# Optimization experiments

Measured on AMD Instinct MI355X. Metric: run time of the kernel, lower is better.

Reference implementation:

```python
import jax, jax.numpy as jnp
import numpy as np

B, S, E, H = 8, 1024, 1024, 16
DK = E // H  # = n_wires = 64


def setup_inputs() -> dict:
    key = jax.random.key(0)
    k1, k2, k3 = jax.random.split(key, 3)
    x = jax.random.normal(k1, (B, S, E), dtype=jnp.float32)
    # trainable per-wire RX angles (shared across tokens and heads, as in QLayer)
    theta = jax.random.normal(k2, (DK,), dtype=jnp.float32)
    # combine_heads: nn.Linear(E, E, bias=False) -> weight [E, E], y = x @ W.T
    W_combine = (jax.random.normal(k3, (E, E), dtype=jnp.float32) / np.float32(np.sqrt(E)))
    return {"x": x, "theta": theta, "W_combine": W_combine}


def reference(x, theta, W_combine):
    # Quantum projection: per wire, RX(x_i) then RX(theta_i) on |0>, measure PauliZ.
    # RX(a)RX(b) = RX(a+b); <Z> of RX(a)|0> = cos(a)  =>  proj = cos(x + theta).
    b, s, e = x.shape
    xh = x.reshape(b, s, H, DK)            # [B, S, H, DK]
    proj = jnp.cos(xh + theta)             # product-state circuit, fully vectorized
    qkv = proj.transpose(0, 2, 1, 3)       # [B, H, S, DK]; q = k = v = proj

    scale = jnp.float32(1.0 / np.sqrt(DK))
    scores = jnp.einsum('bhqd,bhkd->bhqk', qkv, qkv) * scale  # [B, H, S, S]
    attn = jax.nn.softmax(scores, axis=-1)  # dropout disabled (eval / p=0)
    out = jnp.einsum('bhqk,bhkd->bhqd', attn, qkv)            # [B, H, S, DK]
    out = out.transpose(0, 2, 1, 3).reshape(b, s, e)          # [B, S, E]
    return out @ W_combine.T
```

## Files before the change

### kernel.cpp

```cpp
#include <hip/hip_runtime.h>
#include <hip/hip_bf16.h>
#include <stdint.h>

typedef float  f32x4   __attribute__((ext_vector_type(4)));
typedef float  f32x16  __attribute__((ext_vector_type(16)));
typedef __bf16 bf16x8  __attribute__((ext_vector_type(8)));
typedef __bf16 bf16x4  __attribute__((ext_vector_type(4)));

static constexpr int NB = 8, NS = 1024, NE = 1024, NH = 16;

#define MFMA16(a, b, c) __builtin_amdgcn_mfma_f32_16x16x32_bf16((a), (b), (c), 0, 0, 0)
#define MFMA32(a, b, c) __builtin_amdgcn_mfma_f32_32x32x16_bf16((a), (b), (c), 0, 0, 0)

__device__ __forceinline__ void gload_lds16(const void* g, void* l) {
    __builtin_amdgcn_global_load_lds(
        (const __attribute__((address_space(1))) void*)g,
        (__attribute__((address_space(3))) void*)l, 16, 0, 0);
}

__device__ __forceinline__ uint32_t cvt_pk_bf16(float lo, float hi) {
    uint32_t r;
    asm("v_cvt_pk_bf16_f32 %0, %1, %2" : "=v"(r) : "v"(lo), "v"(hi));
    return r;
}
__device__ __forceinline__ void pl32swap(uint32_t& a, uint32_t& b) {
    asm volatile("v_permlane32_swap_b32 %0, %1" : "+v"(a), "+v"(b));
}
__device__ __forceinline__ float exp2_raw(float x) {
    float r;
    asm("v_exp_f32 %0, %1" : "=v"(r) : "v"(x));
    return r;
}

__global__ __launch_bounds__(256) void k_proj(const float* __restrict__ x,
                                              const float* __restrict__ theta,
                                              __bf16* __restrict__ proj,
                                              __bf16* __restrict__ projT) {
    __shared__ float sm[64][65];
    const int bid  = blockIdx.x;
    const int bh   = bid >> 4;
    const int st0  = (bid & 15) << 6;
    const int b    = bh >> 4, h = bh & 15;
    const int t    = threadIdx.x;
    const int srow = t >> 2;
    const int j4   = t & 3;

    const float* xrow = x + ((size_t)(b * NS + st0 + srow)) * NE + h * 64;
    __bf16* prow = proj + ((size_t)bh * NS + st0 + srow) * 64;

#pragma unroll
    for (int k = 0; k < 4; ++k) {
        const int d = k * 16 + j4 * 4;
        float4 xv = *(const float4*)(xrow + d);
        float4 tv = *(const float4*)(theta + d);
        float c0 = __cosf(xv.x + tv.x);
        float c1 = __cosf(xv.y + tv.y);
        float c2 = __cosf(xv.z + tv.z);
        float c3 = __cosf(xv.w + tv.w);
        bf16x4 pv = {(__bf16)c0, (__bf16)c1, (__bf16)c2, (__bf16)c3};
        *(bf16x4*)(prow + d) = pv;
        sm[d + 0][srow] = c0;
        sm[d + 1][srow] = c1;
        sm[d + 2][srow] = c2;
        sm[d + 3][srow] = c3;
    }
    __syncthreads();

    const int drow = t >> 2;
    bf16x8 o0, o1;
#pragma unroll
    for (int i = 0; i < 8; ++i) {
        o0[i] = (__bf16)sm[drow][j4 * 16 + i];
        o1[i] = (__bf16)sm[drow][j4 * 16 + 8 + i];
    }
    __bf16* dst = projT + ((size_t)bh * 64 + drow) * NS + st0 + j4 * 16;
    *(bf16x8*)dst = o0;
    *(bf16x8*)(dst + 8) = o1;
}

__global__ __launch_bounds__(256) void k_cvtW(const float* __restrict__ W,
                                              __bf16* __restrict__ Wb) {
    const int i = (blockIdx.x * 256 + threadIdx.x) * 4;
    float4 v = *(const float4*)(W + i);
    bf16x4 o = {(__bf16)v.x, (__bf16)v.y, (__bf16)v.z, (__bf16)v.w};
    *(bf16x4*)(Wb + i) = o;
}

__global__ __launch_bounds__(256, 2) void k_attn(const __bf16* __restrict__ proj,
                                                 const __bf16* __restrict__ projT,
                                                 __bf16* __restrict__ attn_out) {
    __shared__ __align__(16) char smem[49152];
    __bf16* const smK0 = (__bf16*)(smem);
    __bf16* const smV0 = (__bf16*)(smem + 8192);
    __bf16* const smK1 = (__bf16*)(smem + 16384);
    __bf16* const smV1 = (__bf16*)(smem + 24576);
    __bf16* const smK2 = (__bf16*)(smem + 32768);
    __bf16* const smV2 = (__bf16*)(smem + 40960);

    const int bid  = blockIdx.x;
    const int bh   = (bid & 7) + 8 * ((bid >> 3) & 15);
    const int qblk = bid >> 7;
    const int t    = threadIdx.x;
    const int w    = t >> 6;
    const int lane = t & 63;
    const int hi   = lane >> 5;
    const int l5   = lane & 31;
    const int l7   = l5 & 7;
    const int qw   = qblk * 256 + w * 64;
    const int b    = bh >> 4, h = bh & 15;

    const __bf16* P  = proj  + (size_t)bh * NS * 64;
    const __bf16* PT = projT + (size_t)bh * 64 * NS;

    const float csc = 0.18033688f;

    bf16x8 bq[2][4];
#pragma unroll
    for (int q01 = 0; q01 < 2; ++q01)
#pragma unroll
        for (int d = 0; d < 4; ++d)
            bq[q01][d] = *(const bf16x8*)(P + (size_t)(qw + q01 * 32 + l5) * 64 + d * 16 + hi * 8);

    int roff[4];
#pragma unroll
    for (int d = 0; d < 4; ++d) roff[d] = l5 * 64 + ((d * 2 + hi) ^ l7) * 8;

    const int srow  = t >> 3;
    const int sjsrc = (t & 7) ^ (srow & 7);
    char* const sdK0 = (char*)smK0 + t * 16;
    char* const sdV0 = (char*)smV0 + t * 16;
    char* const sdK1 = (char*)smK1 + t * 16;
    char* const sdV1 = (char*)smV1 + t * 16;
    char* const sdK2 = (char*)smK2 + t * 16;
    char* const sdV2 = (char*)smV2 + t * 16;

#define STAGE(kvoff, dk, dv)                                                           \
    do {                                                                               \
        gload_lds16(P  + (size_t)((kvoff) + srow)      * 64 + sjsrc * 8, (dk));        \
        gload_lds16(P  + (size_t)((kvoff) + 32 + srow) * 64 + sjsrc * 8, (dk) + 4096); \
        gload_lds16(PT + (size_t)srow        * NS + (kvoff) + sjsrc * 8, (dv));        \
        gload_lds16(PT + (size_t)(32 + srow) * NS + (kvoff) + sjsrc * 8, (dv) + 4096); \
    } while (0)

    f32x16 acc0[2], acc1[2];
#pragma unroll
    for (int dt = 0; dt < 2; ++dt) {
        acc0[dt] = (f32x16){0.f,0.f,0.f,0.f,0.f,0.f,0.f,0.f,0.f,0.f,0.f,0.f,0.f,0.f,0.f,0.f};
        acc1[dt] = (f32x16){0.f,0.f,0.f,0.f,0.f,0.f,0.f,0.f,0.f,0.f,0.f,0.f,0.f,0.f,0.f,0.f};
    }
    float rs0 = 0.f, rs1 = 0.f;

    auto computeTile = [&](const __bf16* kB, const __bf16* vB) {
#pragma unroll
        for (int kt = 0; kt < 2; ++kt) {
            bf16x8 ak[4];
#pragma unroll
            for (int d = 0; d < 4; ++d)
                ak[d] = *(const bf16x8*)(kB + roff[d] + kt * 2048);

            f32x16 st0 = (f32x16){0.f,0.f,0.f,0.f,0.f,0.f,0.f,0.f,0.f,0.f,0.f,0.f,0.f,0.f,0.f,0.f};
            f32x16 st1 = (f32x16){0.f,0.f,0.f,0.f,0.f,0.f,0.f,0.f,0.f,0.f,0.f,0.f,0.f,0.f,0.f,0.f};
            __builtin_amdgcn_s_setprio(1);
#pragma unroll
            for (int d = 0; d < 4; ++d) {
                st0 = MFMA32(ak[d], bq[0][d], st0);
                st1 = MFMA32(ak[d], bq[1][d], st1);
            }
            __builtin_amdgcn_s_setprio(0);

            uint32_t c0[8], c1[8];
            {
                float p[16];
#pragma unroll
                for (int r = 0; r < 16; ++r) p[r] = exp2_raw(st0[r] * csc);
                rs0 += (((p[0] + p[1]) + (p[2] + p[3])) + ((p[4] + p[5]) + (p[6] + p[7]))) +
                       (((p[8] + p[9]) + (p[10] + p[11])) + ((p[12] + p[13]) + (p[14] + p[15])));
#pragma unroll
                for (int j = 0; j < 8; ++j) c0[j] = cvt_pk_bf16(p[2 * j], p[2 * j + 1]);
            }
            {
                float p[16];
#pragma unroll
                for (int r = 0; r < 16; ++r) p[r] = exp2_raw(st1[r] * csc);
                rs1 += (((p[0] + p[1]) + (p[2] + p[3])) + ((p[4] + p[5]) + (p[6] + p[7]))) +
                       (((p[8] + p[9]) + (p[10] + p[11])) + ((p[12] + p[13]) + (p[14] + p[15])));
#pragma unroll
                for (int j = 0; j < 8; ++j) c1[j] = cvt_pk_bf16(p[2 * j], p[2 * j + 1]);
            }
            pl32swap(c0[0], c0[2]); pl32swap(c0[1], c0[3]);
            pl32swap(c0[4], c0[6]); pl32swap(c0[5], c0[7]);
            pl32swap(c1[0], c1[2]); pl32swap(c1[1], c1[3]);
            pl32swap(c1[4], c1[6]); pl32swap(c1[5], c1[7]);

#pragma unroll
            for (int half = 0; half < 2; ++half) {
                const int ks = kt * 2 + half;
                union U4 { uint32_t u[4]; bf16x8 v; };
                U4 f0, f1;
#pragma unroll
                for (int j = 0; j < 4; ++j) {
                    f0.u[j] = c0[half * 4 + j];
                    f1.u[j] = c1[half * 4 + j];
                }
                __builtin_amdgcn_s_setprio(1);
#pragma unroll
                for (int dt = 0; dt < 2; ++dt) {
                    bf16x8 av = *(const bf16x8*)(vB + roff[ks] + dt * 2048);
                    acc0[dt] = MFMA32(av, f0.v, acc0[dt]);
                    acc1[dt] = MFMA32(av, f1.v, acc1[dt]);
                }
                __builtin_amdgcn_s_setprio(0);
            }
        }
    };

#define PHASE(IT, CUR, NXT, WAITN)                                        \
    do {                                                                  \
        asm volatile("s_waitcnt vmcnt(" #WAITN ")" ::: "memory");         \
        __builtin_amdgcn_sched_barrier(0);                                \
        __builtin_amdgcn_s_barrier();                                     \
        __builtin_amdgcn_sched_barrier(0);                                \
        if ((IT) < 14) STAGE(((IT) + 2) * 64, sdK##NXT, sdV##NXT);        \
        computeTile(smK##CUR, smV##CUR);                                  \
    } while (0)

    STAGE(0, sdK0, sdV0);
    STAGE(64, sdK1, sdV1);

#pragma unroll 1
    for (int g3 = 0; g3 < 5; ++g3) {
        const int it0 = g3 * 3;
        PHASE(it0 + 0, 0, 2, 4);
        PHASE(it0 + 1, 1, 0, 4);
        PHASE(it0 + 2, 2, 1, 4);
    }
    PHASE(15, 0, 2, 0);

#undef PHASE
#undef STAGE

    __builtin_amdgcn_sched_barrier(0);
    __builtin_amdgcn_s_barrier();

    float* const epw = (float*)smem + w * (32 * 33);
    const int orow = lane >> 1;
    const int ohalf = lane & 1;

#pragma unroll
    for (int q01 = 0; q01 < 2; ++q01) {
        float rs = (q01 == 0) ? rs0 : rs1;
        rs += __shfl_xor(rs, 32);
        const float inv = 1.0f / rs;
#pragma unroll
        for (int dt = 0; dt < 2; ++dt) {
            const f32x16 a = (q01 == 0) ? acc0[dt] : acc1[dt];
#pragma unroll
            for (int r = 0; r < 16; ++r)
                epw[l5 * 33 + (r & 3) + 8 * (r >> 2) + 4 * hi] = a[r] * inv;
            bf16x8 o0, o1;
#pragma unroll
            for (int i = 0; i < 8; ++i) {
                o0[i] = (__bf16)(epw[orow * 33 + ohalf * 16 + i]);
                o1[i] = (__bf16)(epw[orow * 33 + ohalf * 16 + 8 + i]);
            }
            __bf16* dst = attn_out +
                ((size_t)b * NS + qblk * 256 + w * 64 + q01 * 32 + orow) * NE +
                h * 64 + dt * 32 + ohalf * 16;
            *(bf16x8*)dst = o0;
            *(bf16x8*)(dst + 8) = o1;
        }
    }
}

__global__ __launch_bounds__(256) void k_gemm(const __bf16* __restrict__ A,
                                              const __bf16* __restrict__ Bw,
                                              float* __restrict__ C) {
    constexpr int K = 1024, N = 1024;
    __shared__ __bf16 As[128 * 32];
    __shared__ __bf16 Bs[128 * 32];

    const int t = threadIdx.x;
    const int lane = t & 63, w = t >> 6;
    const int g = lane >> 4, c = lane & 15;
    const int wr = w >> 1, wc = w & 1;
    const size_t row0 = (size_t)blockIdx.x * 128;
    const size_t col0 = (size_t)blockIdx.y * 128;

    const char* Ag = (const char*)(A + row0 * K);
    const char* Bg = (const char*)(Bw + col0 * K);
    char* AsB = (char*)As;
    char* BsB = (char*)Bs;
    const int srow  = t >> 2;
    const int sbyte = (t & 3) * 16;

    f32x4 acc[4][4];
#pragma unroll
    for (int m = 0; m < 4; ++m)
#pragma unroll
        for (int n = 0; n < 4; ++n) acc[m][n] = (f32x4){0.f, 0.f, 0.f, 0.f};

    for (int kb = 0; kb < K; kb += 32) {
        gload_lds16(Ag + (size_t)srow * (K * 2) + kb * 2 + sbyte, AsB + t * 16);
        gload_lds16(Ag + (size_t)(srow + 64) * (K * 2) + kb * 2 + sbyte, AsB + 4096 + t * 16);
        gload_lds16(Bg + (size_t)srow * (K * 2) + kb * 2 + sbyte, BsB + t * 16);
        gload_lds16(Bg + (size_t)(srow + 64) * (K * 2) + kb * 2 + sbyte, BsB + 4096 + t * 16);
        __syncthreads();

        bf16x8 a[4], b[4];
#pragma unroll
        for (int m = 0; m < 4; ++m)
            a[m] = *(const bf16x8*)(As + (wr * 64 + m * 16 + c) * 32 + g * 8);
#pragma unroll
        for (int n = 0; n < 4; ++n)
            b[n] = *(const bf16x8*)(Bs + (wc * 64 + n * 16 + c) * 32 + g * 8);
#pragma unroll
        for (int m = 0; m < 4; ++m)
#pragma unroll
            for (int n = 0; n < 4; ++n) acc[m][n] = MFMA16(a[m], b[n], acc[m][n]);
        __syncthreads();
    }

#pragma unroll
    for (int m = 0; m < 4; ++m)
#pragma unroll
        for (int n = 0; n < 4; ++n)
#pragma unroll
            for (int r = 0; r < 4; ++r)
                C[(row0 + wr * 64 + m * 16 + 4 * g + r) * N + col0 + wc * 64 + n * 16 + c] =
                    acc[m][n][r];
}

extern "C" void kernel_launch(void* const* d_in, const int* in_sizes, int n_in,
                              void* d_out, int out_size, void* d_ws, size_t ws_size,
                              hipStream_t stream) {
    const float* x     = (const float*)d_in[0];
    const float* theta = (const float*)d_in[1];
    const float* W     = (const float*)d_in[2];
    float* out = (float*)d_out;

    char* ws = (char*)d_ws;
    __bf16* proj  = (__bf16*)(ws);
    __bf16* projT = (__bf16*)(ws + 16777216);
    __bf16* Wb    = (__bf16*)(ws + 33554432);
    __bf16* ao    = (__bf16*)(ws + 35651584);

    k_proj<<<NB * NH * (NS / 64), 256, 0, stream>>>(x, theta, proj, projT);
    k_cvtW<<<(NE * NE / 4) / 256, 256, 0, stream>>>(W, Wb);
    k_attn<<<NB * NH * 4, 256, 0, stream>>>(proj, projT, ao);
    dim3 gg(NB * NS / 128, NE / 128);
    k_gemm<<<gg, 256, 0, stream>>>(ao, Wb, out);
}
```

Before: 99.39 us.

## Double KV tile to 128 rows and switch to double-buffered LDS staging

Each attention pipeline step now stages 128 keys/values instead of 64, using two 32 KB LDS buffers instead of three 16 KB buffers. The V tile layout and swizzle offsets are widened to match. The hand-tuned vmcnt waits and triple-buffer rotation are replaced with a simpler stage-next/compute-current loop separated by __syncthreads. The intent is to halve the number of barriers and grow the work per sync, at the cost of a shallower prefetch and a full memory wait at every barrier. LDS use per block also rises to 64 KB.

```diff
diff --git a/kernel.cpp b/kernel.cpp
--- a/kernel.cpp
+++ b/kernel.cpp
@@ -89,13 +89,11 @@
 __global__ __launch_bounds__(256, 2) void k_attn(const __bf16* __restrict__ proj,
                                                  const __bf16* __restrict__ projT,
                                                  __bf16* __restrict__ attn_out) {
-    __shared__ __align__(16) char smem[49152];
+    __shared__ __align__(16) char smem[65536];
     __bf16* const smK0 = (__bf16*)(smem);
-    __bf16* const smV0 = (__bf16*)(smem + 8192);
-    __bf16* const smK1 = (__bf16*)(smem + 16384);
-    __bf16* const smV1 = (__bf16*)(smem + 24576);
-    __bf16* const smK2 = (__bf16*)(smem + 32768);
-    __bf16* const smV2 = (__bf16*)(smem + 40960);
+    __bf16* const smV0 = (__bf16*)(smem + 16384);
+    __bf16* const smK1 = (__bf16*)(smem + 32768);
+    __bf16* const smV1 = (__bf16*)(smem + 49152);
 
     const int bid  = blockIdx.x;
     const int bh   = (bid & 7) + 8 * ((bid >> 3) & 15);
@@ -121,25 +119,31 @@
         for (int d = 0; d < 4; ++d)
             bq[q01][d] = *(const bf16x8*)(P + (size_t)(qw + q01 * 32 + l5) * 64 + d * 16 + hi * 8);
 
-    int roff[4];
-#pragma unroll
-    for (int d = 0; d < 4; ++d) roff[d] = l5 * 64 + ((d * 2 + hi) ^ l7) * 8;
-
-    const int srow  = t >> 3;
-    const int sjsrc = (t & 7) ^ (srow & 7);
-    char* const sdK0 = (char*)smK0 + t * 16;
-    char* const sdV0 = (char*)smV0 + t * 16;
-    char* const sdK1 = (char*)smK1 + t * 16;
-    char* const sdV1 = (char*)smV1 + t * 16;
-    char* const sdK2 = (char*)smK2 + t * 16;
-    char* const sdV2 = (char*)smV2 + t * 16;
-
-#define STAGE(kvoff, dk, dv)                                                           \
-    do {                                                                               \
-        gload_lds16(P  + (size_t)((kvoff) + srow)      * 64 + sjsrc * 8, (dk));        \
-        gload_lds16(P  + (size_t)((kvoff) + 32 + srow) * 64 + sjsrc * 8, (dk) + 4096); \
-        gload_lds16(PT + (size_t)srow        * NS + (kvoff) + sjsrc * 8, (dv));        \
-        gload_lds16(PT + (size_t)(32 + srow) * NS + (kvoff) + sjsrc * 8, (dv) + 4096); \
+    int roffK[4], roffV[8];
+#pragma unroll
+    for (int d = 0; d < 4; ++d) roffK[d] = l5 * 64 + ((d * 2 + hi) ^ l7) * 8;
+#pragma unroll
+    for (int ks = 0; ks < 8; ++ks) roffV[ks] = l5 * 128 + ((ks * 2 + hi) ^ l7) * 8;
+
+    const int srowK = t >> 3;
+    const int sjK   = (t & 7) ^ (srowK & 7);
+    const int srowV = t >> 4;
+    const int sjV   = (t & 15) ^ (srowV & 7);
+    char* const dK0 = (char*)smK0 + t * 16;
+    char* const dV0 = (char*)smV0 + t * 16;
+    char* const dK1 = (char*)smK1 + t * 16;
+    char* const dV1 = (char*)smV1 + t * 16;
+
+#define STAGE(kvoff, dk, dv)                                                             \
+    do {                                                                                 \
+        gload_lds16(P + (size_t)((kvoff) + srowK) * 64 + sjK * 8, (dk));                 \
+        gload_lds16(P + (size_t)((kvoff) + 32 + srowK) * 64 + sjK * 8, (dk) + 4096);     \
+        gload_lds16(P + (size_t)((kvoff) + 64 + srowK) * 64 + sjK * 8, (dk) + 8192);     \
+        gload_lds16(P + (size_t)((kvoff) + 96 + srowK) * 64 + sjK * 8, (dk) + 12288);    \
+        gload_lds16(PT + (size_t)srowV * NS + (kvoff) + sjV * 8, (dv));                  \
+        gload_lds16(PT + (size_t)(16 + srowV) * NS + (kvoff) + sjV * 8, (dv) + 4096);    \
+        gload_lds16(PT + (size_t)(32 + srowV) * NS + (kvoff) + sjV * 8, (dv) + 8192);    \
+        gload_lds16(PT + (size_t)(48 + srowV) * NS + (kvoff) + sjV * 8, (dv) + 12288);   \
     } while (0)
 
     f32x16 acc0[2], acc1[2];
@@ -152,11 +156,11 @@
 
     auto computeTile = [&](const __bf16* kB, const __bf16* vB) {
 #pragma unroll
-        for (int kt = 0; kt < 2; ++kt) {
+        for (int kt = 0; kt < 4; ++kt) {
             bf16x8 ak[4];
 #pragma unroll
             for (int d = 0; d < 4; ++d)
-                ak[d] = *(const bf16x8*)(kB + roff[d] + kt * 2048);
+                ak[d] = *(const bf16x8*)(kB + roffK[d] + kt * 2048);
 
             f32x16 st0 = (f32x16){0.f,0.f,0.f,0.f,0.f,0.f,0.f,0.f,0.f,0.f,0.f,0.f,0.f,0.f,0.f,0.f};
             f32x16 st1 = (f32x16){0.f,0.f,0.f,0.f,0.f,0.f,0.f,0.f,0.f,0.f,0.f,0.f,0.f,0.f,0.f,0.f};
@@ -205,7 +209,7 @@
                 __builtin_amdgcn_s_setprio(1);
 #pragma unroll
                 for (int dt = 0; dt < 2; ++dt) {
-                    bf16x8 av = *(const bf16x8*)(vB + roff[ks] + dt * 2048);
+                    bf16x8 av = *(const bf16x8*)(vB + roffV[ks] + dt * 4096);
                     acc0[dt] = MFMA32(av, f0.v, acc0[dt]);
                     acc1[dt] = MFMA32(av, f1.v, acc1[dt]);
                 }
@@ -214,33 +218,19 @@
         }
     };
 
-#define PHASE(IT, CUR, NXT, WAITN)                                        \
-    do {                                                                  \
-        asm volatile("s_waitcnt vmcnt(" #WAITN ")" ::: "memory");         \
-        __builtin_amdgcn_sched_barrier(0);                                \
-        __builtin_amdgcn_s_barrier();                                     \
-        __builtin_amdgcn_sched_barrier(0);                                \
-        if ((IT) < 14) STAGE(((IT) + 2) * 64, sdK##NXT, sdV##NXT);        \
-        computeTile(smK##CUR, smV##CUR);                                  \
-    } while (0)
-
-    STAGE(0, sdK0, sdV0);
-    STAGE(64, sdK1, sdV1);
+    STAGE(0, dK0, dV0);
+    __syncthreads();
 
 #pragma unroll 1
-    for (int g3 = 0; g3 < 5; ++g3) {
-        const int it0 = g3 * 3;
-        PHASE(it0 + 0, 0, 2, 4);
-        PHASE(it0 + 1, 1, 0, 4);
-        PHASE(it0 + 2, 2, 1, 4);
-    }
-    PHASE(15, 0, 2, 0);
-
-#undef PHASE
+    for (int it2 = 0; it2 < 4; ++it2) {
+        STAGE((2 * it2 + 1) * 128, dK1, dV1);
+        computeTile(smK0, smV0);
+        __syncthreads();
+        if (it2 < 3) STAGE((2 * it2 + 2) * 128, dK0, dV0);
+        computeTile(smK1, smV1);
+        __syncthreads();
+    }
 #undef STAGE
-
-    __builtin_amdgcn_sched_barrier(0);
-    __builtin_amdgcn_s_barrier();
 
     float* const epw = (float*)smem + w * (32 * 33);
     const int orow = lane >> 1;
```

Result: slower. 114.8 us (+15.5%).

## Double-buffer GEMM with swizzled 64-wide K tiles; simplify attention pipeline to two buffers

Applied to the files above, without the earlier changes.

The output-projection GEMM now uses double-buffered 128x64 LDS tiles with an XOR swizzle, staging the next K tile while computing the current one. This is meant to hide global-load latency and cut barrier count and LDS bank conflicts. The attention kernel drops from a three-buffer, vmcnt-controlled pipeline to a two-buffer scheme synchronized with __syncthreads, which shrinks its LDS footprint but waits on all outstanding loads at every barrier. The k_cvtW launch is also reordered ahead of k_proj.

```diff
diff --git a/kernel.cpp b/kernel.cpp
--- a/kernel.cpp
+++ b/kernel.cpp
@@ -89,13 +89,11 @@
 __global__ __launch_bounds__(256, 2) void k_attn(const __bf16* __restrict__ proj,
                                                  const __bf16* __restrict__ projT,
                                                  __bf16* __restrict__ attn_out) {
-    __shared__ __align__(16) char smem[49152];
+    __shared__ __align__(16) char smem[32768];
     __bf16* const smK0 = (__bf16*)(smem);
     __bf16* const smV0 = (__bf16*)(smem + 8192);
     __bf16* const smK1 = (__bf16*)(smem + 16384);
     __bf16* const smV1 = (__bf16*)(smem + 24576);
-    __bf16* const smK2 = (__bf16*)(smem + 32768);
-    __bf16* const smV2 = (__bf16*)(smem + 40960);
 
     const int bid  = blockIdx.x;
     const int bh   = (bid & 7) + 8 * ((bid >> 3) & 15);
@@ -127,12 +125,10 @@
 
     const int srow  = t >> 3;
     const int sjsrc = (t & 7) ^ (srow & 7);
-    char* const sdK0 = (char*)smK0 + t * 16;
-    char* const sdV0 = (char*)smV0 + t * 16;
-    char* const sdK1 = (char*)smK1 + t * 16;
-    char* const sdV1 = (char*)smV1 + t * 16;
-    char* const sdK2 = (char*)smK2 + t * 16;
-    char* const sdV2 = (char*)smV2 + t * 16;
+    char* const dK0 = (char*)smK0 + t * 16;
+    char* const dV0 = (char*)smV0 + t * 16;
+    char* const dK1 = (char*)smK1 + t * 16;
+    char* const dV1 = (char*)smV1 + t * 16;
 
 #define STAGE(kvoff, dk, dv)                                                           \
     do {                                                                               \
@@ -214,33 +210,19 @@
         }
     };
 
-#define PHASE(IT, CUR, NXT, WAITN)                                        \
-    do {                                                                  \
-        asm volatile("s_waitcnt vmcnt(" #WAITN ")" ::: "memory");         \
-        __builtin_amdgcn_sched_barrier(0);                                \
-        __builtin_amdgcn_s_barrier();                                     \
-        __builtin_amdgcn_sched_barrier(0);                                \
-        if ((IT) < 14) STAGE(((IT) + 2) * 64, sdK##NXT, sdV##NXT);        \
-        computeTile(smK##CUR, smV##CUR);                                  \
-    } while (0)
-
-    STAGE(0, sdK0, sdV0);
-    STAGE(64, sdK1, sdV1);
+    STAGE(0, dK0, dV0);
+    __syncthreads();
 
 #pragma unroll 1
-    for (int g3 = 0; g3 < 5; ++g3) {
-        const int it0 = g3 * 3;
-        PHASE(it0 + 0, 0, 2, 4);
-        PHASE(it0 + 1, 1, 0, 4);
-        PHASE(it0 + 2, 2, 1, 4);
-    }
-    PHASE(15, 0, 2, 0);
-
-#undef PHASE
+    for (int it2 = 0; it2 < 8; ++it2) {
+        STAGE((2 * it2 + 1) * 64, dK1, dV1);
+        computeTile(smK0, smV0);
+        __syncthreads();
+        if (it2 < 7) STAGE((2 * it2 + 2) * 64, dK0, dV0);
+        computeTile(smK1, smV1);
+        __syncthreads();
+    }
 #undef STAGE
-
-    __builtin_amdgcn_sched_barrier(0);
-    __builtin_amdgcn_s_barrier();
 
     float* const epw = (float*)smem + w * (32 * 33);
     const int orow = lane >> 1;
@@ -272,12 +254,12 @@
     }
 }
 
-__global__ __launch_bounds__(256) void k_gemm(const __bf16* __restrict__ A,
-                                              const __bf16* __restrict__ Bw,
-                                              float* __restrict__ C) {
+__global__ __launch_bounds__(256, 2) void k_gemm(const __bf16* __restrict__ A,
+                                                 const __bf16* __restrict__ Bw,
+                                                 float* __restrict__ C) {
     constexpr int K = 1024, N = 1024;
-    __shared__ __bf16 As[128 * 32];
-    __shared__ __bf16 Bs[128 * 32];
+    __shared__ __align__(16) __bf16 As[2][128 * 64];
+    __shared__ __align__(16) __bf16 Bs[2][128 * 64];
 
     const int t = threadIdx.x;
     const int lane = t & 63, w = t >> 6;
@@ -286,12 +268,22 @@
     const size_t row0 = (size_t)blockIdx.x * 128;
     const size_t col0 = (size_t)blockIdx.y * 128;
 
-    const char* Ag = (const char*)(A + row0 * K);
-    const char* Bg = (const char*)(Bw + col0 * K);
-    char* AsB = (char*)As;
-    char* BsB = (char*)Bs;
-    const int srow  = t >> 2;
-    const int sbyte = (t & 3) * 16;
+    const __bf16* Ag = A  + row0 * K;
+    const __bf16* Bg = Bw + col0 * K;
+
+    const int srow = t >> 3;
+    const int sj   = (t & 7) ^ (srow & 7);
+
+#define GSTAGE(kb, buf)                                                           \
+    do {                                                                          \
+        _Pragma("unroll")                                                         \
+        for (int p = 0; p < 4; ++p) {                                             \
+            gload_lds16(Ag + (size_t)(p * 32 + srow) * K + (kb) + sj * 8,         \
+                        (char*)&As[buf][0] + p * 4096 + t * 16);                  \
+            gload_lds16(Bg + (size_t)(p * 32 + srow) * K + (kb) + sj * 8,         \
+                        (char*)&Bs[buf][0] + p * 4096 + t * 16);                  \
+        }                                                                         \
+    } while (0)
 
     f32x4 acc[4][4];
 #pragma unroll
@@ -299,26 +291,40 @@
 #pragma unroll
         for (int n = 0; n < 4; ++n) acc[m][n] = (f32x4){0.f, 0.f, 0.f, 0.f};
 
-    for (int kb = 0; kb < K; kb += 32) {
-        gload_lds16(Ag + (size_t)srow * (K * 2) + kb * 2 + sbyte, AsB + t * 16);
-        gload_lds16(Ag + (size_t)(srow + 64) * (K * 2) + kb * 2 + sbyte, AsB + 4096 + t * 16);
-        gload_lds16(Bg + (size_t)srow * (K * 2) + kb * 2 + sbyte, BsB + t * 16);
-        gload_lds16(Bg + (size_t)(srow + 64) * (K * 2) + kb * 2 + sbyte, BsB + 4096 + t * 16);
+    const int c7 = c & 7;
+
+    auto computeBuf = [&](int buf) {
+#pragma unroll
+        for (int ks = 0; ks < 2; ++ks) {
+            bf16x8 a[4], bfr[4];
+#pragma unroll
+            for (int m = 0; m < 4; ++m)
+                a[m] = *(const bf16x8*)(&As[buf][(wr * 64 + m * 16 + c) * 64 +
+                                                 ((ks * 4 + g) ^ c7) * 8]);
+#pragma unroll
+            for (int n = 0; n < 4; ++n)
+                bfr[n] = *(const bf16x8*)(&Bs[buf][(wc * 64 + n * 16 + c) * 64 +
+                                                   ((ks * 4 + g) ^ c7) * 8]);
+#pragma unroll
+            for (int m = 0; m < 4; ++m)
+#pragma unroll
+                for (int n = 0; n < 4; ++n) acc[m][n] = MFMA16(a[m], bfr[n], acc[m][n]);
+        }
+    };
+
+    GSTAGE(0, 0);
+    __syncthreads();
+
+#pragma unroll 1
+    for (int kt = 0; kt < 8; ++kt) {
+        GSTAGE(kt * 128 + 64, 1);
+        computeBuf(0);
         __syncthreads();
-
-        bf16x8 a[4], b[4];
-#pragma unroll
-        for (int m = 0; m < 4; ++m)
-            a[m] = *(const bf16x8*)(As + (wr * 64 + m * 16 + c) * 32 + g * 8);
-#pragma unroll
-        for (int n = 0; n < 4; ++n)
-            b[n] = *(const bf16x8*)(Bs + (wc * 64 + n * 16 + c) * 32 + g * 8);
-#pragma unroll
-        for (int m = 0; m < 4; ++m)
-#pragma unroll
-            for (int n = 0; n < 4; ++n) acc[m][n] = MFMA16(a[m], b[n], acc[m][n]);
+        if (kt < 7) GSTAGE(kt * 128 + 128, 0);
+        computeBuf(1);
         __syncthreads();
     }
+#undef GSTAGE
 
 #pragma unroll
     for (int m = 0; m < 4; ++m)
@@ -344,8 +350,8 @@
     __bf16* Wb    = (__bf16*)(ws + 33554432);
     __bf16* ao    = (__bf16*)(ws + 35651584);
 
+    k_cvtW<<<(NE * NE / 4) / 256, 256, 0, stream>>>(W, Wb);
     k_proj<<<NB * NH * (NS / 64), 256, 0, stream>>>(x, theta, proj, projT);
-    k_cvtW<<<(NE * NE / 4) / 256, 256, 0, stream>>>(W, Wb);
     k_attn<<<NB * NH * 4, 256, 0, stream>>>(proj, projT, ao);
     dim3 gg(NB * NS / 128, NE / 128);
     k_gemm<<<gg, 256, 0, stream>>>(ao, Wb, out);
```

After: 84.47 us. -15.0%, faster.
